# Optimization experiments

Hardware: AMD Instinct MI355X
Metric: run time of the kernel (lower is better)

Reference implementation:

```python
import jax, jax.numpy as jnp
import numpy as np

D = 2048  # input_dim == hidden_dim (mult=1)
B = 16
C = 8.0   # self.c


def setup_inputs() -> dict:
    key = jax.random.key(0)
    k = jax.random.split(key, 5)
    # kaiming_normal fan_in, sigmoid gain = 1 -> std = 1/sqrt(fan_in)
    Wa = jax.random.normal(k[0], (D, D), dtype=jnp.float32) / np.sqrt(D)
    Wx = jax.random.normal(k[1], (D, D), dtype=jnp.float32) / np.sqrt(D)
    ba = jnp.zeros((D,), dtype=jnp.float32)
    bx = jnp.zeros((D,), dtype=jnp.float32)
    lo, hi = float(np.log(0.9 / 0.1)), float(np.log(0.999 / 0.001))  # logit(0.9), logit(0.999)
    Lam = jax.random.uniform(k[2], (D,), dtype=jnp.float32, minval=lo, maxval=hi)
    xt = jax.random.normal(k[3], (B, D), dtype=jnp.float32)
    ht_minus_1 = jax.random.normal(k[4], (B, D), dtype=jnp.float32)
    return {"xt": xt, "ht_minus_1": ht_minus_1, "Wa": Wa, "Wx": Wx,
            "ba": ba, "bx": bx, "Lam": Lam}


def reference(xt, ht_minus_1, Wa, Wx, ba, bx, Lam):
    # gates
    rt = jax.nn.sigmoid(xt @ Wa.T + ba)            # [B, H]
    it = jax.nn.sigmoid(xt @ Wx.T + bx)            # [B, H]
    log_a = -jax.nn.softplus(-Lam)                 # [H]
    a = jnp.exp(log_a * rt / C)                    # [B, H]
    # diag_embed(a): [B, H, H] with a on the diagonal (faithful to torch code)
    at = a[:, :, None] * jnp.eye(D, dtype=a.dtype)
    u = jnp.sqrt(1.0 - a * a) * (it * xt)          # [B, H]
    # torch broadcasting: [B,H,H] * [B,H] -> ht_minus_1/u broadcast over rows
    ht = at * ht_minus_1[:, None, :] + u[:, None, :]  # [B, H, H]
    return ht
```

## Files before the change

### kernel.cpp

```cpp
#include <hip/hip_runtime.h>

#define DD 2048
#define BB 16

typedef float f32x4 __attribute__((ext_vector_type(4)));
typedef short bf16x8 __attribute__((ext_vector_type(8)));

static __device__ inline short f2bf(float f) {
    unsigned u = __builtin_bit_cast(unsigned, f);
    return (short)((u + 0x7fffu + ((u >> 16) & 1u)) >> 16);
}

static __device__ inline bf16x8 cvt8(f32x4 a, f32x4 b) {
    bf16x8 r;
#pragma unroll
    for (int e = 0; e < 4; ++e) {
        r[e]     = f2bf(a[e]);
        r[4 + e] = f2bf(b[e]);
    }
    return r;
}

__global__ __launch_bounds__(512) void gemm_kernel(
    const float* __restrict__ xt,
    const float* __restrict__ Wa, const float* __restrict__ Wx,
    float* __restrict__ rawA, float* __restrict__ rawX)
{
    const int gate = blockIdx.x & 1;
    const int jt   = blockIdx.x >> 1;
    const int wv   = threadIdx.x >> 6;
    const int lane = threadIdx.x & 63;
    const int mn   = lane & 15;
    const int kc   = lane >> 4;

    const float* W = gate ? Wx : Wa;
    const float* wrow = W  + (size_t)(jt * 16 + mn) * DD;
    const float* xrow = xt + (size_t)mn * DD;
    const int kbase = wv * 256 + kc * 8;

    f32x4 acc = {0.f, 0.f, 0.f, 0.f};
#pragma unroll
    for (int s = 0; s < 8; ++s) {
        const int k = kbase + s * 32;
        const f32x4 wa0 = *(const f32x4*)(wrow + k);
        const f32x4 wa1 = *(const f32x4*)(wrow + k + 4);
        const f32x4 xb0 = *(const f32x4*)(xrow + k);
        const f32x4 xb1 = *(const f32x4*)(xrow + k + 4);
        const bf16x8 af = cvt8(wa0, wa1);
        const bf16x8 bf_ = cvt8(xb0, xb1);
        acc = __builtin_amdgcn_mfma_f32_16x16x32_bf16(af, bf_, acc, 0, 0, 0);
    }

    __shared__ float part[8][256];
#pragma unroll
    for (int r = 0; r < 4; ++r) part[wv][lane * 4 + r] = acc[r];
    __syncthreads();

    if (threadIdx.x < 256) {
        const int t = threadIdx.x;
        float s = 0.f;
#pragma unroll
        for (int w = 0; w < 8; ++w) s += part[w][t];
        const int l   = t >> 2;
        const int r   = t & 3;
        const int row = ((l >> 4) << 2) + r;
        const int col = l & 15;
        float* dst = gate ? rawX : rawA;
        dst[col * DD + jt * 16 + row] = s;
    }
}

__global__ __launch_bounds__(256) void finalize_kernel(
    const float* __restrict__ xt, const float* __restrict__ h,
    const float* __restrict__ ba, const float* __restrict__ bx,
    const float* __restrict__ Lam,
    float* __restrict__ rawA_u, float* __restrict__ rawX_dv)
{
    const int g = blockIdx.x * 256 + threadIdx.x;
    const int b = g >> 11;
    const int j = g & (DD - 1);

    const float sA = rawA_u[g] + ba[j];
    const float sX = rawX_dv[g] + bx[j];
    const float rt  = 1.f / (1.f + expf(-sA));
    const float itg = 1.f / (1.f + expf(-sX));
    const float log_a = -log1pf(expf(-Lam[j]));
    const float a = expf(log_a * rt * 0.125f);
    const float u = sqrtf(fmaxf(0.f, 1.f - a * a)) * (itg * xt[b * DD + j]);
    const float dv = fmaf(a, h[b * DD + j], u);
    rawA_u[g]  = u;
    rawX_dv[g] = dv;
}

__global__ __launch_bounds__(256) void fill_kernel(
    const float4* __restrict__ u4, const float* __restrict__ dv,
    float4* __restrict__ out)
{
    const int blk = blockIdx.x;
    const int b   = blk >> 8;
    const int ig  = blk & 255;
    const int i0  = ig << 3;
    const int t   = threadIdx.x;

    const float4 v0 = u4[(b << 9) + t];
    const float4 v1 = u4[(b << 9) + 256 + t];

    float4* orow = out + ((size_t)b << 20) + ((size_t)i0 << 9);
#pragma unroll
    for (int r = 0; r < 8; ++r) {
        const int i   = i0 + r;
        const int dj4 = i >> 2;
        float4 w0 = v0, w1 = v1;
        if (dj4 == t) {
            ((float*)&w0)[i & 3] = dv[(b << 11) + i];
        } else if (dj4 == 256 + t) {
            ((float*)&w1)[i & 3] = dv[(b << 11) + i];
        }
        orow[t]       = w0;
        orow[256 + t] = w1;
        orow += DD / 4;
    }
}

extern "C" void kernel_launch(void* const* d_in, const int* in_sizes, int n_in,
                              void* d_out, int out_size, void* d_ws, size_t ws_size,
                              hipStream_t stream) {
    const float* xt  = (const float*)d_in[0];
    const float* h   = (const float*)d_in[1];
    const float* Wa  = (const float*)d_in[2];
    const float* Wx  = (const float*)d_in[3];
    const float* ba  = (const float*)d_in[4];
    const float* bx  = (const float*)d_in[5];
    const float* Lam = (const float*)d_in[6];

    float* ws0 = (float*)d_ws;
    float* ws1 = ws0 + BB * DD;

    gemm_kernel<<<256, 512, 0, stream>>>(xt, Wa, Wx, ws0, ws1);
    finalize_kernel<<<BB * DD / 256, 256, 0, stream>>>(xt, h, ba, bx, Lam, ws0, ws1);
    fill_kernel<<<BB * (DD / 8), 256, 0, stream>>>((const float4*)ws0, ws1, (float4*)d_out);
}
```

Before: 61.66 us.

## Fuse gate finalize into fill kernel and fold bias into GEMM epilogue

Removes the separate finalize kernel: the bias add moves into the GEMM epilogue and the sigmoid/decay/u/dv math is recomputed per block inside the fill kernel. The fill grid shrinks from 4096 to 512 blocks, each writing 64 output rows instead of 8, which amortizes the per-block gate computation. bf16 conversion now uses the compiler's native cast. This saves one launch and a workspace round trip, in exchange for fewer, longer fill blocks on a store-bound 268MB output.

```diff
diff --git a/kernel.cpp b/kernel.cpp
--- a/kernel.cpp
+++ b/kernel.cpp
@@ -6,24 +6,27 @@
 typedef float f32x4 __attribute__((ext_vector_type(4)));
 typedef short bf16x8 __attribute__((ext_vector_type(8)));
 
-static __device__ inline short f2bf(float f) {
-    unsigned u = __builtin_bit_cast(unsigned, f);
-    return (short)((u + 0x7fffu + ((u >> 16) & 1u)) >> 16);
+static __device__ inline short bfbits(float f) {
+    __bf16 h = (__bf16)f;
+    return __builtin_bit_cast(short, h);
 }
 
 static __device__ inline bf16x8 cvt8(f32x4 a, f32x4 b) {
     bf16x8 r;
 #pragma unroll
     for (int e = 0; e < 4; ++e) {
-        r[e]     = f2bf(a[e]);
-        r[4 + e] = f2bf(b[e]);
+        r[e]     = bfbits(a[e]);
+        r[4 + e] = bfbits(b[e]);
     }
     return r;
 }
 
+static __device__ inline float sigmoidf_(float s) { return 1.f / (1.f + expf(-s)); }
+
 __global__ __launch_bounds__(512) void gemm_kernel(
     const float* __restrict__ xt,
     const float* __restrict__ Wa, const float* __restrict__ Wx,
+    const float* __restrict__ ba, const float* __restrict__ bx,
     float* __restrict__ rawA, float* __restrict__ rawX)
 {
     const int gate = blockIdx.x & 1;
@@ -46,7 +49,7 @@
         const f32x4 wa1 = *(const f32x4*)(wrow + k + 4);
         const f32x4 xb0 = *(const f32x4*)(xrow + k);
         const f32x4 xb1 = *(const f32x4*)(xrow + k + 4);
-        const bf16x8 af = cvt8(wa0, wa1);
+        const bf16x8 af  = cvt8(wa0, wa1);
         const bf16x8 bf_ = cvt8(xb0, xb1);
         acc = __builtin_amdgcn_mfma_f32_16x16x32_bf16(af, bf_, acc, 0, 0, 0);
     }
@@ -65,56 +68,55 @@
         const int r   = t & 3;
         const int row = ((l >> 4) << 2) + r;
         const int col = l & 15;
-        float* dst = gate ? rawX : rawA;
-        dst[col * DD + jt * 16 + row] = s;
+        const int j   = jt * 16 + row;
+        s += (gate ? bx : ba)[j];
+        (gate ? rawX : rawA)[col * DD + j] = s;
     }
 }
 
-__global__ __launch_bounds__(256) void finalize_kernel(
+__global__ __launch_bounds__(256) void fill_kernel(
     const float* __restrict__ xt, const float* __restrict__ h,
-    const float* __restrict__ ba, const float* __restrict__ bx,
+    const float* __restrict__ rawA, const float* __restrict__ rawX,
     const float* __restrict__ Lam,
-    float* __restrict__ rawA_u, float* __restrict__ rawX_dv)
-{
-    const int g = blockIdx.x * 256 + threadIdx.x;
-    const int b = g >> 11;
-    const int j = g & (DD - 1);
-
-    const float sA = rawA_u[g] + ba[j];
-    const float sX = rawX_dv[g] + bx[j];
-    const float rt  = 1.f / (1.f + expf(-sA));
-    const float itg = 1.f / (1.f + expf(-sX));
-    const float log_a = -log1pf(expf(-Lam[j]));
-    const float a = expf(log_a * rt * 0.125f);
-    const float u = sqrtf(fmaxf(0.f, 1.f - a * a)) * (itg * xt[b * DD + j]);
-    const float dv = fmaf(a, h[b * DD + j], u);
-    rawA_u[g]  = u;
-    rawX_dv[g] = dv;
-}
-
-__global__ __launch_bounds__(256) void fill_kernel(
-    const float4* __restrict__ u4, const float* __restrict__ dv,
     float4* __restrict__ out)
 {
     const int blk = blockIdx.x;
-    const int b   = blk >> 8;
-    const int ig  = blk & 255;
-    const int i0  = ig << 3;
+    const int b   = blk >> 5;
+    const int ig  = blk & 31;
+    const int i0  = ig << 6;
     const int t   = threadIdx.x;
 
-    const float4 v0 = u4[(b << 9) + t];
-    const float4 v1 = u4[(b << 9) + 256 + t];
+    float4 u[2], dvv[2];
+#pragma unroll
+    for (int hh = 0; hh < 2; ++hh) {
+        const int j0 = hh * 1024 + t * 4;
+        const f32x4 sa  = *(const f32x4*)(rawA + b * DD + j0);
+        const f32x4 sx  = *(const f32x4*)(rawX + b * DD + j0);
+        const f32x4 xv  = *(const f32x4*)(xt   + b * DD + j0);
+        const f32x4 hv  = *(const f32x4*)(h    + b * DD + j0);
+        const f32x4 lam = *(const f32x4*)(Lam + j0);
+#pragma unroll
+        for (int e = 0; e < 4; ++e) {
+            const float rt  = sigmoidf_(sa[e]);
+            const float itg = sigmoidf_(sx[e]);
+            const float log_a = -log1pf(expf(-lam[e]));
+            const float a = expf(log_a * rt * 0.125f);
+            const float uu = sqrtf(fmaxf(0.f, 1.f - a * a)) * (itg * xv[e]);
+            ((float*)&u[hh])[e]   = uu;
+            ((float*)&dvv[hh])[e] = fmaf(a, hv[e], uu);
+        }
+    }
 
     float4* orow = out + ((size_t)b << 20) + ((size_t)i0 << 9);
-#pragma unroll
-    for (int r = 0; r < 8; ++r) {
+#pragma unroll 8
+    for (int r = 0; r < 64; ++r) {
         const int i   = i0 + r;
         const int dj4 = i >> 2;
-        float4 w0 = v0, w1 = v1;
+        float4 w0 = u[0], w1 = u[1];
         if (dj4 == t) {
-            ((float*)&w0)[i & 3] = dv[(b << 11) + i];
+            ((float*)&w0)[i & 3] = ((const float*)&dvv[0])[i & 3];
         } else if (dj4 == 256 + t) {
-            ((float*)&w1)[i & 3] = dv[(b << 11) + i];
+            ((float*)&w1)[i & 3] = ((const float*)&dvv[1])[i & 3];
         }
         orow[t]       = w0;
         orow[256 + t] = w1;
@@ -133,10 +135,9 @@
     const float* bx  = (const float*)d_in[5];
     const float* Lam = (const float*)d_in[6];
 
-    float* ws0 = (float*)d_ws;
-    float* ws1 = ws0 + BB * DD;
+    float* rawA = (float*)d_ws;
+    float* rawX = rawA + BB * DD;
 
-    gemm_kernel<<<256, 512, 0, stream>>>(xt, Wa, Wx, ws0, ws1);
-    finalize_kernel<<<BB * DD / 256, 256, 0, stream>>>(xt, h, ba, bx, Lam, ws0, ws1);
-    fill_kernel<<<BB * (DD / 8), 256, 0, stream>>>((const float4*)ws0, ws1, (float4*)d_out);
+    gemm_kernel<<<256, 512, 0, stream>>>(xt, Wa, Wx, ba, bx, rawA, rawX);
+    fill_kernel<<<512, 256, 0, stream>>>(xt, h, rawA, rawX, Lam, (float4*)d_out);
 }
```

After: 63.93 us. 1.04x slower.
